# Performance work log

Hardware: AMD Instinct MI355X
Metric: run time of the kernel (lower is better)

Reference implementation:

```python
import jax, jax.numpy as jnp
import numpy as np


def setup_inputs() -> dict:
    key = jax.random.key(0)
    k1, k2 = jax.random.split(key)
    ns, nd, n_classes = 16384, 2048, 1000
    x = jax.random.normal(k1, (ns, nd), dtype=jnp.float32)
    # prototype means for all seen classes (seen_c == n_classes)
    means = jax.random.normal(k2, (n_classes, nd), dtype=jnp.float32)
    return {"x": x, "means": means, "n_classes": n_classes}


def reference(x, means, n_classes):
    # Original: per-sample dist = -means @ x[s]; argmin(dist) == argmax(means @ x[s]).
    # Batched: one GEMM [ns, nd] x [nd, seen_c] -> scores [ns, seen_c].
    ns = x.shape[0]
    xf = x.reshape(ns, -1)
    scores = jnp.einsum('nd,cd->nc', xf, means)  # [ns, seen_c]
    classpred = jnp.argmax(scores, axis=1)       # argmin of -scores
    out = jax.nn.one_hot(classpred, n_classes, dtype=jnp.float32)  # [ns, n_classes]
    return out
```

## Files before the change

kernel.cpp:

```cpp
#include <hip/hip_runtime.h>
#include <math.h>

#define NS 16384
#define ND 2048
#define NC 1000
#define NCPAD 1024

typedef _Float16 f16x8 __attribute__((ext_vector_type(8)));
typedef _Float16 f16x4 __attribute__((ext_vector_type(4)));
typedef __fp16   h16x2 __attribute__((ext_vector_type(2)));
typedef float f32x4  __attribute__((ext_vector_type(4)));

#define DELTA 2.5f

#define WS_NEW 104857600ull
#define WS_MID 37748736ull

__device__ __forceinline__ void gl_lds16_h(const _Float16* g, _Float16* l) {
    __builtin_amdgcn_global_load_lds(
        (const __attribute__((address_space(1))) unsigned int*)g,
        (__attribute__((address_space(3))) unsigned int*)l, 16, 0, 0);
}
__device__ __forceinline__ void gl_lds16_f(const float* g, float* l) {
    __builtin_amdgcn_global_load_lds(
        (const __attribute__((address_space(1))) unsigned int*)g,
        (__attribute__((address_space(3))) unsigned int*)l, 16, 0, 0);
}

__device__ __forceinline__ f16x8 cvt8(const f32x4 a0, const f32x4 a1) {
    const h16x2 h01 = __builtin_amdgcn_cvt_pkrtz(a0[0], a0[1]);
    const h16x2 h23 = __builtin_amdgcn_cvt_pkrtz(a0[2], a0[3]);
    const h16x2 h45 = __builtin_amdgcn_cvt_pkrtz(a1[0], a1[1]);
    const h16x2 h67 = __builtin_amdgcn_cvt_pkrtz(a1[2], a1[3]);
    f16x8 h;
    h[0]=(_Float16)h01[0]; h[1]=(_Float16)h01[1]; h[2]=(_Float16)h23[0]; h[3]=(_Float16)h23[1];
    h[4]=(_Float16)h45[0]; h[5]=(_Float16)h45[1]; h[6]=(_Float16)h67[0]; h[7]=(_Float16)h67[1];
    return h;
}

__global__ __launch_bounds__(256)
void cvt_all_kernel(const float* __restrict__ x, const float* __restrict__ means,
                    _Float16* __restrict__ xh, _Float16* __restrict__ mhi)
{
    const size_t i = (size_t)blockIdx.x * 256 + threadIdx.x;
    const size_t NM4 = (size_t)NCPAD * ND / 4;
    if (i < NM4) {
        const int row = (int)(i >> 9);
        float4 v = make_float4(0.f, 0.f, 0.f, 0.f);
        if (row < NC) v = ((const float4*)means)[i];
        f16x4 h;
        h[0]=(_Float16)v.x; h[1]=(_Float16)v.y; h[2]=(_Float16)v.z; h[3]=(_Float16)v.w;
        ((f16x4*)mhi)[i] = h;
    } else {
        const size_t j = i - NM4;
        const float4 v = ((const float4*)x)[j];
        f16x4 h;
        h[0]=(_Float16)v.x; h[1]=(_Float16)v.y; h[2]=(_Float16)v.z; h[3]=(_Float16)v.w;
        ((f16x4*)xh)[j] = h;
    }
}

__device__ __forceinline__ void stage_unit(const _Float16* __restrict__ src,
                                           size_t g0, _Float16* dstbase,
                                           int ktile, int kkh, int tid)
{
    const int srcT = ktile < 31 ? ktile : 31;
#pragma unroll
    for (int q = 0; q < 2; ++q) {
        const int slot = q * 512 + tid;
        const int row  = slot >> 2;
        const int g    = (slot & 3) ^ ((row >> 1) & 3);
        gl_lds16_h(src + ((g0 + (size_t)row) << 11) + srcT * 64 + kkh * 32 + g * 8,
                   dstbase + (size_t)(q * 512 + ((tid >> 6) << 6)) * 8);
    }
}

__global__ __launch_bounds__(512, 2)
void gemm256_kernel(const _Float16* __restrict__ xh,
                    const _Float16* __restrict__ mhi,
                    _Float16* __restrict__ sc)
{
    __shared__ _Float16 sA[2][2][256 * 32];
    __shared__ _Float16 sB[2][2][256 * 32];

    const int tid  = threadIdx.x;
    const int lane = tid & 63;
    const int w    = tid >> 6;
    const int wm   = w >> 2;
    const int wn   = w & 3;
    const int quad = lane >> 4, l16 = lane & 15;

    const int orig = blockIdx.x + (blockIdx.y << 2);
    const int nid  = ((orig & 7) << 5) + (orig >> 3);
    const size_t gm0 = (size_t)(nid >> 2) * 256;
    const size_t gn0 = (size_t)(nid & 3) * 256;

    f32x4 acc[8][4] = {};

    stage_unit(xh,  gm0, &sA[0][0][0], 0, 0, tid);
    stage_unit(mhi, gn0, &sB[0][0][0], 0, 0, tid);
    stage_unit(xh,  gm0, &sA[0][1][0], 0, 1, tid);
    stage_unit(mhi, gn0, &sB[0][1][0], 0, 1, tid);
    stage_unit(xh,  gm0, &sA[1][0][0], 1, 0, tid);
    stage_unit(mhi, gn0, &sB[1][0][0], 1, 0, tid);
    asm volatile("s_waitcnt vmcnt(4)" ::: "memory");
    __builtin_amdgcn_s_barrier();

    for (int kt = 0; kt < 32; ++kt) {
        const int par = kt & 1;

        f16x8 a0[4], a1[4], b0[4], c0[4], c1[4];
#pragma unroll
        for (int i = 0; i < 4; ++i) {
            const int r0 = wm * 128 + i * 16 + l16;
            const int r1 = r0 + 64;
            const int p0 = quad ^ ((r0 >> 1) & 3);
            const int p1 = quad ^ ((r1 >> 1) & 3);
            a0[i] = *(const f16x8*)&sA[par][0][r0 * 32 + p0 * 8];
            a1[i] = *(const f16x8*)&sA[par][0][r1 * 32 + p1 * 8];
        }
#pragma unroll
        for (int j = 0; j < 4; ++j) {
            const int br = wn * 64 + j * 16 + l16;
            const int pc = quad ^ ((br >> 1) & 3);
            b0[j] = *(const f16x8*)&sB[par][0][br * 32 + pc * 8];
        }
#pragma unroll
        for (int i = 0; i < 4; ++i) {
            const int r0 = wm * 128 + i * 16 + l16;
            const int r1 = r0 + 64;
            const int p0 = quad ^ ((r0 >> 1) & 3);
            const int p1 = quad ^ ((r1 >> 1) & 3);
            c0[i] = *(const f16x8*)&sA[par][1][r0 * 32 + p0 * 8];
            c1[i] = *(const f16x8*)&sA[par][1][r1 * 32 + p1 * 8];
        }
        stage_unit(xh,  gm0, &sA[(kt + 1) & 1][1][0], kt + 1, 1, tid);
        stage_unit(mhi, gn0, &sB[(kt + 1) & 1][1][0], kt + 1, 1, tid);
        __builtin_amdgcn_sched_barrier(0);
        __builtin_amdgcn_s_setprio(1);
#pragma unroll
        for (int i = 0; i < 4; ++i)
#pragma unroll
            for (int j = 0; j < 4; ++j)
                acc[i][j] = __builtin_amdgcn_mfma_f32_16x16x32_f16(a0[i], b0[j], acc[i][j], 0, 0, 0);
#pragma unroll
        for (int i = 0; i < 4; ++i)
#pragma unroll
            for (int j = 0; j < 4; ++j)
                acc[4 + i][j] = __builtin_amdgcn_mfma_f32_16x16x32_f16(a1[i], b0[j], acc[4 + i][j], 0, 0, 0);
        __builtin_amdgcn_s_setprio(0);
        __builtin_amdgcn_s_barrier();

        f16x8 b1[4];
#pragma unroll
        for (int j = 0; j < 4; ++j) {
            const int br = wn * 64 + j * 16 + l16;
            const int pc = quad ^ ((br >> 1) & 3);
            b1[j] = *(const f16x8*)&sB[par][1][br * 32 + pc * 8];
        }
        stage_unit(xh,  gm0, &sA[par][0][0], kt + 2, 0, tid);
        stage_unit(mhi, gn0, &sB[par][0][0], kt + 2, 0, tid);
        __builtin_amdgcn_sched_barrier(0);
        __builtin_amdgcn_s_setprio(1);
#pragma unroll
        for (int i = 0; i < 4; ++i)
#pragma unroll
            for (int j = 0; j < 4; ++j)
                acc[i][j] = __builtin_amdgcn_mfma_f32_16x16x32_f16(c0[i], b1[j], acc[i][j], 0, 0, 0);
#pragma unroll
        for (int i = 0; i < 4; ++i)
#pragma unroll
            for (int j = 0; j < 4; ++j)
                acc[4 + i][j] = __builtin_amdgcn_mfma_f32_16x16x32_f16(c1[i], b1[j], acc[4 + i][j], 0, 0, 0);
        __builtin_amdgcn_s_setprio(0);
        asm volatile("s_waitcnt vmcnt(4)" ::: "memory");
        __builtin_amdgcn_s_barrier();
    }

#pragma unroll
    for (int m = 0; m < 8; ++m) {
        const size_t row0 = gm0 + wm * 128 + m * 16 + quad * 4;
#pragma unroll
        for (int j = 0; j < 4; ++j) {
            const size_t col = gn0 + wn * 64 + j * 16 + l16;
#pragma unroll
            for (int r = 0; r < 4; ++r)
                sc[(row0 + r) * NCPAD + col] = (_Float16)acc[m][j][r];
        }
    }
}

__global__ __launch_bounds__(512, 4)
void gemm_f32a_kernel(const float* __restrict__ x,
                      const _Float16* __restrict__ mhi,
                      _Float16* __restrict__ sc)
{
    __shared__ float    sA [128 * 32];
    __shared__ _Float16 sBh[256 * 32];

    const int tid  = threadIdx.x;
    const int lane = tid & 63;
    const int w    = tid >> 6;
    const int wm   = w & 1;
    const int wn   = w >> 1;
    const int quad = lane >> 4, l16 = lane & 15;
    const size_t gm0 = (size_t)blockIdx.y * 128;
    const size_t gn0 = (size_t)blockIdx.x * 256;

    f32x4 acc[4][4] = {};

    for (int kt = 0; kt < ND / 32; ++kt) {
        const int k0 = kt * 32;
#pragma unroll
        for (int r = 0; r < 2; ++r) {
            const int slot = r * 512 + tid;
            const int arow = slot >> 3;
            const int ac   = (slot & 7) ^ (arow & 7);
            gl_lds16_f(x + ((gm0 + arow) << 11) + k0 + ac * 4,
                       &sA[(r * 512 + w * 64) * 4]);
            const int brow = slot >> 2;
            const int bc   = (slot & 3) ^ ((brow >> 1) & 3);
            gl_lds16_h(mhi + ((gn0 + brow) << 11) + k0 + bc * 8,
                       &sBh[(r * 512 + w * 64) * 8]);
        }
        __syncthreads();

        f16x8 ah[4], bh[4];
#pragma unroll
        for (int i = 0; i < 4; ++i) {
            const int ar = wm * 64 + i * 16 + l16;
            const int c1 = (2 * quad)     ^ (ar & 7);
            const int c2 = (2 * quad + 1) ^ (ar & 7);
            const f32x4 a0 = *(const f32x4*)&sA[ar * 32 + c1 * 4];
            const f32x4 a1 = *(const f32x4*)&sA[ar * 32 + c2 * 4];
            ah[i] = cvt8(a0, a1);
        }
#pragma unroll
        for (int j = 0; j < 4; ++j) {
            const int br = wn * 64 + j * 16 + l16;
            const int pc = quad ^ ((br >> 1) & 3);
            bh[j] = *(const f16x8*)&sBh[br * 32 + pc * 8];
        }
#pragma unroll
        for (int i = 0; i < 4; ++i)
#pragma unroll
            for (int j = 0; j < 4; ++j)
                acc[i][j] = __builtin_amdgcn_mfma_f32_16x16x32_f16(ah[i], bh[j], acc[i][j], 0, 0, 0);
        __syncthreads();
    }

#pragma unroll
    for (int i = 0; i < 4; ++i) {
        const size_t row0 = gm0 + wm * 64 + i * 16 + quad * 4;
#pragma unroll
        for (int j = 0; j < 4; ++j) {
            const size_t col = gn0 + wn * 64 + j * 16 + l16;
#pragma unroll
            for (int r = 0; r < 4; ++r)
                sc[(row0 + r) * NCPAD + col] = (_Float16)acc[i][j][r];
        }
    }
}

__global__ __launch_bounds__(256)
void cvt_m_kernel(const float* __restrict__ src, _Float16* __restrict__ hi)
{
    const int i = blockIdx.x * 256 + threadIdx.x;
    const int row = (i * 4) >> 11;
    float4 v = make_float4(0.f, 0.f, 0.f, 0.f);
    if (row < NC) v = ((const float4*)src)[i];
    f16x4 h;
    h[0] = (_Float16)v.x; h[1] = (_Float16)v.y;
    h[2] = (_Float16)v.z; h[3] = (_Float16)v.w;
    ((f16x4*)hi)[i] = h;
}

__global__ __launch_bounds__(256, 4)
void refine_kernel(const _Float16* __restrict__ sc,
                   const float* __restrict__ x,
                   const float* __restrict__ means,
                   float* __restrict__ out)
{
    const int lane = threadIdx.x & 63;
    const int row  = blockIdx.x * 4 + (threadIdx.x >> 6);

    const f16x8* srow = (const f16x8*)(sc + (size_t)row * NCPAD + lane * 16);
    const f16x8 s0 = srow[0], s1 = srow[1];
    float v[16];
#pragma unroll
    for (int e = 0; e < 8; ++e) { v[e] = (float)s0[e]; v[8 + e] = (float)s1[e]; }

    float mx = -INFINITY;
#pragma unroll
    for (int e = 0; e < 16; ++e) {
        const int c = lane * 16 + e;
        if (c < NC && v[e] > mx) mx = v[e];
    }
#pragma unroll
    for (int off = 1; off < 64; off <<= 1) {
        const float o = __shfl_xor(mx, off);
        if (o > mx) mx = o;
    }
    const float T = mx - DELTA;

    unsigned cm = 0;
#pragma unroll
    for (int e = 0; e < 16; ++e) {
        const int c = lane * 16 + e;
        if (c < NC && v[e] >= T) cm |= (1u << e);
    }

    const unsigned long long bl = __ballot(cm != 0u);
    const int first  = (int)__builtin_ctzll(bl);
    const unsigned cmf = (unsigned)__shfl((int)cm, first);

    int bc;
    if (__builtin_popcountll(bl) == 1 && __builtin_popcount(cmf) == 1) {
        bc = first * 16 + __builtin_ctz(cmf);
    } else {
        const float* xrow = x + ((size_t)row << 11);
        f32x4 xr[8];
#pragma unroll
        for (int it = 0; it < 8; ++it)
            xr[it] = *(const f32x4*)(xrow + it * 256 + lane * 4);

        float bv = -INFINITY;
        bc = 0x7fffffff;
        unsigned long long pend = bl;
        while (pend) {
            const int src = (int)__builtin_ctzll(pend);
            pend &= pend - 1;
            unsigned cms = (unsigned)__shfl((int)cm, src);
            while (cms) {
                const int c = src * 16 + __builtin_ctz(cms);
                cms &= cms - 1;

                const float* mrow = means + ((size_t)c << 11);
                float part = 0.f;
#pragma unroll
                for (int it = 0; it < 8; ++it) {
                    const f32x4 mv = *(const f32x4*)(mrow + it * 256 + lane * 4);
                    part = fmaf(xr[it][0], mv[0], part);
                    part = fmaf(xr[it][1], mv[1], part);
                    part = fmaf(xr[it][2], mv[2], part);
                    part = fmaf(xr[it][3], mv[3], part);
                }
                float s = part;
#pragma unroll
                for (int off = 1; off < 64; off <<= 1) s += __shfl_xor(s, off);

                if (s > bv || (s == bv && c < bc)) { bv = s; bc = c; }
            }
        }
    }

    float4* orow = (float4*)(out + (size_t)row * NC);
#pragma unroll
    for (int i = 0; i < 4; ++i) {
        const int idx = lane + i * 64;
        if (idx < NC / 4) {
            const int cb = idx * 4;
            float4 ov;
            ov.x = (cb     == bc) ? 1.f : 0.f;
            ov.y = (cb + 1 == bc) ? 1.f : 0.f;
            ov.z = (cb + 2 == bc) ? 1.f : 0.f;
            ov.w = (cb + 3 == bc) ? 1.f : 0.f;
            orow[idx] = ov;
        }
    }
}

#define MS 64
#define CS 256
#define KT 32
#define NCHUNK 4

__global__ __launch_bounds__(256, 1)
void nnc_fp32_kernel(const float* __restrict__ x,
                     const float* __restrict__ means,
                     float* __restrict__ out)
{
    __shared__ float xs[MS * KT];
    __shared__ float msh[CS * KT];
    __shared__ float rbest[MS * 33];
    __shared__ int   ridx[MS * 33];
    __shared__ int   widx[MS];

    const int tid = threadIdx.x;
    const int tx  = tid & 31;
    const int ty  = tid >> 5;
    const int s0  = blockIdx.x * MS;
    const int m0  = ty * 8;
    const int cL  = tx * 8;

    float best[8];
    int   bidx[8];
#pragma unroll
    for (int i = 0; i < 8; ++i) { best[i] = -INFINITY; bidx[i] = 0; }

    const int kslot = tid & 7;
    const int rrow  = tid >> 3;

    for (int chunk = 0; chunk < NCHUNK; ++chunk) {
        const int c0 = chunk * CS;
        float acc[8][8];
#pragma unroll
        for (int i = 0; i < 8; ++i)
#pragma unroll
            for (int j = 0; j < 8; ++j) acc[i][j] = 0.0f;

        for (int k0 = 0; k0 < ND; k0 += KT) {
#pragma unroll
            for (int r = 0; r < 2; ++r) {
                const int m = rrow + r * 32;
                const float4 v = *(const float4*)(x + (size_t)(s0 + m) * ND + k0 + kslot * 4);
                *(float4*)(xs + m * KT + kslot * 4) = v;
            }
#pragma unroll
            for (int r = 0; r < 8; ++r) {
                const int c  = rrow + r * 32;
                const int cg = c0 + c;
                float4 v = make_float4(0.f, 0.f, 0.f, 0.f);
                if (cg < NC) v = *(const float4*)(means + (size_t)cg * ND + k0 + kslot * 4);
                const int pslot = (kslot + (c >> 3)) & 7;
                *(float4*)(msh + c * KT + pslot * 4) = v;
            }
            __syncthreads();
#pragma unroll
            for (int k4 = 0; k4 < KT / 4; ++k4) {
                float4 a[8], b[8];
                const int boff = ((k4 + tx) & 7) * 4;
#pragma unroll
                for (int i = 0; i < 8; ++i) a[i] = *(const float4*)(xs + (m0 + i) * KT + k4 * 4);
#pragma unroll
                for (int j = 0; j < 8; ++j) b[j] = *(const float4*)(msh + (cL + j) * KT + boff);
#pragma unroll
                for (int i = 0; i < 8; ++i)
#pragma unroll
                    for (int j = 0; j < 8; ++j) {
                        acc[i][j] = fmaf(a[i].x, b[j].x, acc[i][j]);
                        acc[i][j] = fmaf(a[i].y, b[j].y, acc[i][j]);
                        acc[i][j] = fmaf(a[i].z, b[j].z, acc[i][j]);
                        acc[i][j] = fmaf(a[i].w, b[j].w, acc[i][j]);
                    }
            }
            __syncthreads();
        }
#pragma unroll
        for (int i = 0; i < 8; ++i)
#pragma unroll
            for (int j = 0; j < 8; ++j) {
                const int c = c0 + cL + j;
                const float v = acc[i][j];
                if (c < NC && (v > best[i] || (v == best[i] && c < bidx[i]))) {
                    best[i] = v; bidx[i] = c;
                }
            }
    }
#pragma unroll
    for (int i = 0; i < 8; ++i) {
        rbest[(m0 + i) * 33 + tx] = best[i];
        ridx[(m0 + i) * 33 + tx]  = bidx[i];
    }
    __syncthreads();
    if (tid < MS) {
        float bv = rbest[tid * 33];
        int   bc = ridx[tid * 33];
        for (int t = 1; t < 32; ++t) {
            const float v = rbest[tid * 33 + t];
            const int   c = ridx[tid * 33 + t];
            if (v > bv || (v == bv && c < bc)) { bv = v; bc = c; }
        }
        widx[tid] = bc;
    }
    __syncthreads();
    if (tid < 250) {
        const int cbase = tid * 4;
        for (int m = 0; m < MS; ++m) {
            const int w = widx[m];
            float4 v;
            v.x = (cbase == w) ? 1.f : 0.f;
            v.y = (cbase + 1 == w) ? 1.f : 0.f;
            v.z = (cbase + 2 == w) ? 1.f : 0.f;
            v.w = (cbase + 3 == w) ? 1.f : 0.f;
            *(float4*)(out + (size_t)(s0 + m) * NC + cbase) = v;
        }
    }
}

extern "C" void kernel_launch(void* const* d_in, const int* in_sizes, int n_in,
                              void* d_out, int out_size, void* d_ws, size_t ws_size,
                              hipStream_t stream) {
    const float* x     = (const float*)d_in[0];
    const float* means = (const float*)d_in[1];
    float* out         = (float*)d_out;

    if (ws_size >= WS_NEW) {
        char* ws = (char*)d_ws;
        _Float16* mhi = (_Float16*)ws;
        _Float16* xh  = (_Float16*)(ws + (4ull  << 20));
        _Float16* sc  = (_Float16*)(ws + (68ull << 20));

        cvt_all_kernel<<<dim3((NCPAD * ND / 4 + NS * ND / 4) / 256), dim3(256), 0, stream>>>(x, means, xh, mhi);
        gemm256_kernel<<<dim3(NCPAD / 256, NS / 256), dim3(512), 0, stream>>>(xh, mhi, sc);
        refine_kernel<<<dim3(NS / 4), dim3(256), 0, stream>>>(sc, x, means, out);
    } else if (ws_size >= WS_MID) {
        char* ws = (char*)d_ws;
        _Float16* mhi = (_Float16*)ws;
        _Float16* sc  = (_Float16*)(ws + 4194304ull);

        cvt_m_kernel<<<dim3(NCPAD * ND / 4 / 256), dim3(256), 0, stream>>>(means, mhi);
        gemm_f32a_kernel<<<dim3(NCPAD / 256, NS / 128), dim3(512), 0, stream>>>(x, mhi, sc);
        refine_kernel<<<dim3(NS / 4), dim3(256), 0, stream>>>(sc, x, means, out);
    } else {
        nnc_fp32_kernel<<<dim3(NS / MS), dim3(256), 0, stream>>>(x, means, out);
    }
}
```

Baseline: 301.8 us.

## Fuse fp32-to-fp16 conversion of x into the 256x256 GEMM A-tile load

Removes the separate pass that converted all of x to fp16 in workspace. The 256x256 GEMM now loads fp32 x straight from global memory into registers, converts it to fp16 and writes the swizzled tile into LDS, while B still arrives through direct global-to-LDS loads. This saves writing and re-reading a 64 MB fp16 copy of x and needs less workspace. In exchange, the A path costs VGPRs and conversion ALU work inside the MFMA loop, and the loop now waits on vmcnt(0) every iteration instead of keeping loads in flight.

```diff
diff --git a/kernel.cpp b/kernel.cpp
--- a/kernel.cpp
+++ b/kernel.cpp
@@ -13,15 +13,9 @@
 
 #define DELTA 2.5f
 
-#define WS_NEW 104857600ull
-#define WS_MID 37748736ull
+#define WS_FAST 37748736ull
 
 __device__ __forceinline__ void gl_lds16_h(const _Float16* g, _Float16* l) {
-    __builtin_amdgcn_global_load_lds(
-        (const __attribute__((address_space(1))) unsigned int*)g,
-        (__attribute__((address_space(3))) unsigned int*)l, 16, 0, 0);
-}
-__device__ __forceinline__ void gl_lds16_f(const float* g, float* l) {
     __builtin_amdgcn_global_load_lds(
         (const __attribute__((address_space(1))) unsigned int*)g,
         (__attribute__((address_space(3))) unsigned int*)l, 16, 0, 0);
@@ -36,230 +30,6 @@
     h[0]=(_Float16)h01[0]; h[1]=(_Float16)h01[1]; h[2]=(_Float16)h23[0]; h[3]=(_Float16)h23[1];
     h[4]=(_Float16)h45[0]; h[5]=(_Float16)h45[1]; h[6]=(_Float16)h67[0]; h[7]=(_Float16)h67[1];
     return h;
-}
-
-__global__ __launch_bounds__(256)
-void cvt_all_kernel(const float* __restrict__ x, const float* __restrict__ means,
-                    _Float16* __restrict__ xh, _Float16* __restrict__ mhi)
-{
-    const size_t i = (size_t)blockIdx.x * 256 + threadIdx.x;
-    const size_t NM4 = (size_t)NCPAD * ND / 4;
-    if (i < NM4) {
-        const int row = (int)(i >> 9);
-        float4 v = make_float4(0.f, 0.f, 0.f, 0.f);
-        if (row < NC) v = ((const float4*)means)[i];
-        f16x4 h;
-        h[0]=(_Float16)v.x; h[1]=(_Float16)v.y; h[2]=(_Float16)v.z; h[3]=(_Float16)v.w;
-        ((f16x4*)mhi)[i] = h;
-    } else {
-        const size_t j = i - NM4;
-        const float4 v = ((const float4*)x)[j];
-        f16x4 h;
-        h[0]=(_Float16)v.x; h[1]=(_Float16)v.y; h[2]=(_Float16)v.z; h[3]=(_Float16)v.w;
-        ((f16x4*)xh)[j] = h;
-    }
-}
-
-__device__ __forceinline__ void stage_unit(const _Float16* __restrict__ src,
-                                           size_t g0, _Float16* dstbase,
-                                           int ktile, int kkh, int tid)
-{
-    const int srcT = ktile < 31 ? ktile : 31;
-#pragma unroll
-    for (int q = 0; q < 2; ++q) {
-        const int slot = q * 512 + tid;
-        const int row  = slot >> 2;
-        const int g    = (slot & 3) ^ ((row >> 1) & 3);
-        gl_lds16_h(src + ((g0 + (size_t)row) << 11) + srcT * 64 + kkh * 32 + g * 8,
-                   dstbase + (size_t)(q * 512 + ((tid >> 6) << 6)) * 8);
-    }
-}
-
-__global__ __launch_bounds__(512, 2)
-void gemm256_kernel(const _Float16* __restrict__ xh,
-                    const _Float16* __restrict__ mhi,
-                    _Float16* __restrict__ sc)
-{
-    __shared__ _Float16 sA[2][2][256 * 32];
-    __shared__ _Float16 sB[2][2][256 * 32];
-
-    const int tid  = threadIdx.x;
-    const int lane = tid & 63;
-    const int w    = tid >> 6;
-    const int wm   = w >> 2;
-    const int wn   = w & 3;
-    const int quad = lane >> 4, l16 = lane & 15;
-
-    const int orig = blockIdx.x + (blockIdx.y << 2);
-    const int nid  = ((orig & 7) << 5) + (orig >> 3);
-    const size_t gm0 = (size_t)(nid >> 2) * 256;
-    const size_t gn0 = (size_t)(nid & 3) * 256;
-
-    f32x4 acc[8][4] = {};
-
-    stage_unit(xh,  gm0, &sA[0][0][0], 0, 0, tid);
-    stage_unit(mhi, gn0, &sB[0][0][0], 0, 0, tid);
-    stage_unit(xh,  gm0, &sA[0][1][0], 0, 1, tid);
-    stage_unit(mhi, gn0, &sB[0][1][0], 0, 1, tid);
-    stage_unit(xh,  gm0, &sA[1][0][0], 1, 0, tid);
-    stage_unit(mhi, gn0, &sB[1][0][0], 1, 0, tid);
-    asm volatile("s_waitcnt vmcnt(4)" ::: "memory");
-    __builtin_amdgcn_s_barrier();
-
-    for (int kt = 0; kt < 32; ++kt) {
-        const int par = kt & 1;
-
-        f16x8 a0[4], a1[4], b0[4], c0[4], c1[4];
-#pragma unroll
-        for (int i = 0; i < 4; ++i) {
-            const int r0 = wm * 128 + i * 16 + l16;
-            const int r1 = r0 + 64;
-            const int p0 = quad ^ ((r0 >> 1) & 3);
-            const int p1 = quad ^ ((r1 >> 1) & 3);
-            a0[i] = *(const f16x8*)&sA[par][0][r0 * 32 + p0 * 8];
-            a1[i] = *(const f16x8*)&sA[par][0][r1 * 32 + p1 * 8];
-        }
-#pragma unroll
-        for (int j = 0; j < 4; ++j) {
-            const int br = wn * 64 + j * 16 + l16;
-            const int pc = quad ^ ((br >> 1) & 3);
-            b0[j] = *(const f16x8*)&sB[par][0][br * 32 + pc * 8];
-        }
-#pragma unroll
-        for (int i = 0; i < 4; ++i) {
-            const int r0 = wm * 128 + i * 16 + l16;
-            const int r1 = r0 + 64;
-            const int p0 = quad ^ ((r0 >> 1) & 3);
-            const int p1 = quad ^ ((r1 >> 1) & 3);
-            c0[i] = *(const f16x8*)&sA[par][1][r0 * 32 + p0 * 8];
-            c1[i] = *(const f16x8*)&sA[par][1][r1 * 32 + p1 * 8];
-        }
-        stage_unit(xh,  gm0, &sA[(kt + 1) & 1][1][0], kt + 1, 1, tid);
-        stage_unit(mhi, gn0, &sB[(kt + 1) & 1][1][0], kt + 1, 1, tid);
-        __builtin_amdgcn_sched_barrier(0);
-        __builtin_amdgcn_s_setprio(1);
-#pragma unroll
-        for (int i = 0; i < 4; ++i)
-#pragma unroll
-            for (int j = 0; j < 4; ++j)
-                acc[i][j] = __builtin_amdgcn_mfma_f32_16x16x32_f16(a0[i], b0[j], acc[i][j], 0, 0, 0);
-#pragma unroll
-        for (int i = 0; i < 4; ++i)
-#pragma unroll
-            for (int j = 0; j < 4; ++j)
-                acc[4 + i][j] = __builtin_amdgcn_mfma_f32_16x16x32_f16(a1[i], b0[j], acc[4 + i][j], 0, 0, 0);
-        __builtin_amdgcn_s_setprio(0);
-        __builtin_amdgcn_s_barrier();
-
-        f16x8 b1[4];
-#pragma unroll
-        for (int j = 0; j < 4; ++j) {
-            const int br = wn * 64 + j * 16 + l16;
-            const int pc = quad ^ ((br >> 1) & 3);
-            b1[j] = *(const f16x8*)&sB[par][1][br * 32 + pc * 8];
-        }
-        stage_unit(xh,  gm0, &sA[par][0][0], kt + 2, 0, tid);
-        stage_unit(mhi, gn0, &sB[par][0][0], kt + 2, 0, tid);
-        __builtin_amdgcn_sched_barrier(0);
-        __builtin_amdgcn_s_setprio(1);
-#pragma unroll
-        for (int i = 0; i < 4; ++i)
-#pragma unroll
-            for (int j = 0; j < 4; ++j)
-                acc[i][j] = __builtin_amdgcn_mfma_f32_16x16x32_f16(c0[i], b1[j], acc[i][j], 0, 0, 0);
-#pragma unroll
-        for (int i = 0; i < 4; ++i)
-#pragma unroll
-            for (int j = 0; j < 4; ++j)
-                acc[4 + i][j] = __builtin_amdgcn_mfma_f32_16x16x32_f16(c1[i], b1[j], acc[4 + i][j], 0, 0, 0);
-        __builtin_amdgcn_s_setprio(0);
-        asm volatile("s_waitcnt vmcnt(4)" ::: "memory");
-        __builtin_amdgcn_s_barrier();
-    }
-
-#pragma unroll
-    for (int m = 0; m < 8; ++m) {
-        const size_t row0 = gm0 + wm * 128 + m * 16 + quad * 4;
-#pragma unroll
-        for (int j = 0; j < 4; ++j) {
-            const size_t col = gn0 + wn * 64 + j * 16 + l16;
-#pragma unroll
-            for (int r = 0; r < 4; ++r)
-                sc[(row0 + r) * NCPAD + col] = (_Float16)acc[m][j][r];
-        }
-    }
-}
-
-__global__ __launch_bounds__(512, 4)
-void gemm_f32a_kernel(const float* __restrict__ x,
-                      const _Float16* __restrict__ mhi,
-                      _Float16* __restrict__ sc)
-{
-    __shared__ float    sA [128 * 32];
-    __shared__ _Float16 sBh[256 * 32];
-
-    const int tid  = threadIdx.x;
-    const int lane = tid & 63;
-    const int w    = tid >> 6;
-    const int wm   = w & 1;
-    const int wn   = w >> 1;
-    const int quad = lane >> 4, l16 = lane & 15;
-    const size_t gm0 = (size_t)blockIdx.y * 128;
-    const size_t gn0 = (size_t)blockIdx.x * 256;
-
-    f32x4 acc[4][4] = {};
-
-    for (int kt = 0; kt < ND / 32; ++kt) {
-        const int k0 = kt * 32;
-#pragma unroll
-        for (int r = 0; r < 2; ++r) {
-            const int slot = r * 512 + tid;
-            const int arow = slot >> 3;
-            const int ac   = (slot & 7) ^ (arow & 7);
-            gl_lds16_f(x + ((gm0 + arow) << 11) + k0 + ac * 4,
-                       &sA[(r * 512 + w * 64) * 4]);
-            const int brow = slot >> 2;
-            const int bc   = (slot & 3) ^ ((brow >> 1) & 3);
-            gl_lds16_h(mhi + ((gn0 + brow) << 11) + k0 + bc * 8,
-                       &sBh[(r * 512 + w * 64) * 8]);
-        }
-        __syncthreads();
-
-        f16x8 ah[4], bh[4];
-#pragma unroll
-        for (int i = 0; i < 4; ++i) {
-            const int ar = wm * 64 + i * 16 + l16;
-            const int c1 = (2 * quad)     ^ (ar & 7);
-            const int c2 = (2 * quad + 1) ^ (ar & 7);
-            const f32x4 a0 = *(const f32x4*)&sA[ar * 32 + c1 * 4];
-            const f32x4 a1 = *(const f32x4*)&sA[ar * 32 + c2 * 4];
-            ah[i] = cvt8(a0, a1);
-        }
-#pragma unroll
-        for (int j = 0; j < 4; ++j) {
-            const int br = wn * 64 + j * 16 + l16;
-            const int pc = quad ^ ((br >> 1) & 3);
-            bh[j] = *(const f16x8*)&sBh[br * 32 + pc * 8];
-        }
-#pragma unroll
-        for (int i = 0; i < 4; ++i)
-#pragma unroll
-            for (int j = 0; j < 4; ++j)
-                acc[i][j] = __builtin_amdgcn_mfma_f32_16x16x32_f16(ah[i], bh[j], acc[i][j], 0, 0, 0);
-        __syncthreads();
-    }
-
-#pragma unroll
-    for (int i = 0; i < 4; ++i) {
-        const size_t row0 = gm0 + wm * 64 + i * 16 + quad * 4;
-#pragma unroll
-        for (int j = 0; j < 4; ++j) {
-            const size_t col = gn0 + wn * 64 + j * 16 + l16;
-#pragma unroll
-            for (int r = 0; r < 4; ++r)
-                sc[(row0 + r) * NCPAD + col] = (_Float16)acc[i][j][r];
-        }
-    }
 }
 
 __global__ __launch_bounds__(256)
@@ -275,6 +45,160 @@
     ((f16x4*)hi)[i] = h;
 }
 
+__device__ __forceinline__ void stage_unitB(const _Float16* __restrict__ src,
+                                            size_t g0, _Float16* dstbase,
+                                            int srcT, int kkh, int tid)
+{
+#pragma unroll
+    for (int q = 0; q < 2; ++q) {
+        const int slot = q * 512 + tid;
+        const int row  = slot >> 2;
+        const int g    = (slot & 3) ^ ((row >> 1) & 3);
+        gl_lds16_h(src + ((g0 + (size_t)row) << 11) + srcT * 64 + kkh * 32 + g * 8,
+                   dstbase + (size_t)(q * 512 + ((tid >> 6) << 6)) * 8);
+    }
+}
+
+__global__ __launch_bounds__(512, 2)
+void gemm256_kernel(const float* __restrict__ x,
+                    const _Float16* __restrict__ mhi,
+                    _Float16* __restrict__ sc)
+{
+    __shared__ _Float16 sA[2][2][256 * 32];
+    __shared__ _Float16 sB[2][2][256 * 32];
+
+    const int tid  = threadIdx.x;
+    const int lane = tid & 63;
+    const int w    = tid >> 6;
+    const int wm   = w >> 2;
+    const int wn   = w & 3;
+    const int quad = lane >> 4, l16 = lane & 15;
+
+    const int orig = blockIdx.x + (blockIdx.y << 2);
+    const int nid  = ((orig & 7) << 5) + (orig >> 3);
+    const size_t gm0 = (size_t)(nid >> 2) * 256;
+    const size_t gn0 = (size_t)(nid & 3) * 256;
+
+    const int arow = tid >> 1;
+    const int aseg = tid & 1;
+    const int as   = (arow >> 1) & 3;
+    const int ap0  = (aseg * 2)     ^ as;
+    const int ap1  = (aseg * 2 + 1) ^ as;
+    const float* xA = x + ((gm0 + (size_t)arow) << 11) + aseg * 16;
+
+    f32x4 acc[8][4] = {};
+
+    stage_unitB(mhi, gn0, &sB[0][0][0], 0, 0, tid);
+    stage_unitB(mhi, gn0, &sB[0][1][0], 0, 1, tid);
+    {
+        f32x4 v0[4], v1[4];
+#pragma unroll
+        for (int q = 0; q < 4; ++q) v0[q] = *(const f32x4*)(xA + q * 4);
+#pragma unroll
+        for (int q = 0; q < 4; ++q) v1[q] = *(const f32x4*)(xA + 32 + q * 4);
+        const f16x8 h00 = cvt8(v0[0], v0[1]), h01 = cvt8(v0[2], v0[3]);
+        const f16x8 h10 = cvt8(v1[0], v1[1]), h11 = cvt8(v1[2], v1[3]);
+        *(f16x8*)&sA[0][0][arow * 32 + ap0 * 8] = h00;
+        *(f16x8*)&sA[0][0][arow * 32 + ap1 * 8] = h01;
+        *(f16x8*)&sA[0][1][arow * 32 + ap0 * 8] = h10;
+        *(f16x8*)&sA[0][1][arow * 32 + ap1 * 8] = h11;
+    }
+    asm volatile("s_waitcnt vmcnt(0) lgkmcnt(0)" ::: "memory");
+    __builtin_amdgcn_s_barrier();
+
+    for (int kt = 0; kt < 32; ++kt) {
+        const int par = kt & 1, nxt = par ^ 1;
+        const int srcT = (kt + 1 < 32) ? kt + 1 : 31;
+        const float* xT = xA + srcT * 64;
+
+        f16x8 a0[4], a1[4], b0[4];
+#pragma unroll
+        for (int i = 0; i < 4; ++i) {
+            const int r0 = wm * 128 + i * 16 + l16;
+            const int r1 = r0 + 64;
+            a0[i] = *(const f16x8*)&sA[par][0][r0 * 32 + (quad ^ ((r0 >> 1) & 3)) * 8];
+            a1[i] = *(const f16x8*)&sA[par][0][r1 * 32 + (quad ^ ((r1 >> 1) & 3)) * 8];
+        }
+#pragma unroll
+        for (int j = 0; j < 4; ++j) {
+            const int br = wn * 64 + j * 16 + l16;
+            b0[j] = *(const f16x8*)&sB[par][0][br * 32 + (quad ^ ((br >> 1) & 3)) * 8];
+        }
+        stage_unitB(mhi, gn0, &sB[nxt][0][0], srcT, 0, tid);
+        stage_unitB(mhi, gn0, &sB[nxt][1][0], srcT, 1, tid);
+        f32x4 av0[4];
+#pragma unroll
+        for (int q = 0; q < 4; ++q) av0[q] = *(const f32x4*)(xT + q * 4);
+        __builtin_amdgcn_sched_barrier(0);
+        __builtin_amdgcn_s_setprio(1);
+#pragma unroll
+        for (int i = 0; i < 4; ++i)
+#pragma unroll
+            for (int j = 0; j < 4; ++j)
+                acc[i][j] = __builtin_amdgcn_mfma_f32_16x16x32_f16(a0[i], b0[j], acc[i][j], 0, 0, 0);
+#pragma unroll
+        for (int i = 0; i < 4; ++i)
+#pragma unroll
+            for (int j = 0; j < 4; ++j)
+                acc[4 + i][j] = __builtin_amdgcn_mfma_f32_16x16x32_f16(a1[i], b0[j], acc[4 + i][j], 0, 0, 0);
+        __builtin_amdgcn_s_setprio(0);
+
+        f16x8 c0[4], c1[4], b1[4];
+#pragma unroll
+        for (int i = 0; i < 4; ++i) {
+            const int r0 = wm * 128 + i * 16 + l16;
+            const int r1 = r0 + 64;
+            c0[i] = *(const f16x8*)&sA[par][1][r0 * 32 + (quad ^ ((r0 >> 1) & 3)) * 8];
+            c1[i] = *(const f16x8*)&sA[par][1][r1 * 32 + (quad ^ ((r1 >> 1) & 3)) * 8];
+        }
+#pragma unroll
+        for (int j = 0; j < 4; ++j) {
+            const int br = wn * 64 + j * 16 + l16;
+            b1[j] = *(const f16x8*)&sB[par][1][br * 32 + (quad ^ ((br >> 1) & 3)) * 8];
+        }
+        {
+            const f16x8 h0 = cvt8(av0[0], av0[1]), h1 = cvt8(av0[2], av0[3]);
+            *(f16x8*)&sA[nxt][0][arow * 32 + ap0 * 8] = h0;
+            *(f16x8*)&sA[nxt][0][arow * 32 + ap1 * 8] = h1;
+        }
+        f32x4 av1[4];
+#pragma unroll
+        for (int q = 0; q < 4; ++q) av1[q] = *(const f32x4*)(xT + 32 + q * 4);
+        __builtin_amdgcn_sched_barrier(0);
+        __builtin_amdgcn_s_setprio(1);
+#pragma unroll
+        for (int i = 0; i < 4; ++i)
+#pragma unroll
+            for (int j = 0; j < 4; ++j)
+                acc[i][j] = __builtin_amdgcn_mfma_f32_16x16x32_f16(c0[i], b1[j], acc[i][j], 0, 0, 0);
+#pragma unroll
+        for (int i = 0; i < 4; ++i)
+#pragma unroll
+            for (int j = 0; j < 4; ++j)
+                acc[4 + i][j] = __builtin_amdgcn_mfma_f32_16x16x32_f16(c1[i], b1[j], acc[4 + i][j], 0, 0, 0);
+        __builtin_amdgcn_s_setprio(0);
+        {
+            const f16x8 h0 = cvt8(av1[0], av1[1]), h1 = cvt8(av1[2], av1[3]);
+            *(f16x8*)&sA[nxt][1][arow * 32 + ap0 * 8] = h0;
+            *(f16x8*)&sA[nxt][1][arow * 32 + ap1 * 8] = h1;
+        }
+        asm volatile("s_waitcnt vmcnt(0) lgkmcnt(0)" ::: "memory");
+        __builtin_amdgcn_s_barrier();
+    }
+
+#pragma unroll
+    for (int m = 0; m < 8; ++m) {
+        const size_t row0 = gm0 + wm * 128 + m * 16 + quad * 4;
+#pragma unroll
+        for (int j = 0; j < 4; ++j) {
+            const size_t col = gn0 + wn * 64 + j * 16 + l16;
+#pragma unroll
+            for (int r = 0; r < 4; ++r)
+                sc[(row0 + r) * NCPAD + col] = (_Float16)acc[m][j][r];
+        }
+    }
+}
+
 __global__ __launch_bounds__(256, 4)
 void refine_kernel(const _Float16* __restrict__ sc,
                    const float* __restrict__ x,
@@ -495,22 +419,13 @@
     const float* means = (const float*)d_in[1];
     float* out         = (float*)d_out;
 
-    if (ws_size >= WS_NEW) {
+    if (ws_size >= WS_FAST) {
         char* ws = (char*)d_ws;
         _Float16* mhi = (_Float16*)ws;
-        _Float16* xh  = (_Float16*)(ws + (4ull  << 20));
-        _Float16* sc  = (_Float16*)(ws + (68ull << 20));
-
-        cvt_all_kernel<<<dim3((NCPAD * ND / 4 + NS * ND / 4) / 256), dim3(256), 0, stream>>>(x, means, xh, mhi);
-        gemm256_kernel<<<dim3(NCPAD / 256, NS / 256), dim3(512), 0, stream>>>(xh, mhi, sc);
-        refine_kernel<<<dim3(NS / 4), dim3(256), 0, stream>>>(sc, x, means, out);
-    } else if (ws_size >= WS_MID) {
-        char* ws = (char*)d_ws;
-        _Float16* mhi = (_Float16*)ws;
-        _Float16* sc  = (_Float16*)(ws + 4194304ull);
+        _Float16* sc  = (_Float16*)(ws + (4ull << 20));
 
         cvt_m_kernel<<<dim3(NCPAD * ND / 4 / 256), dim3(256), 0, stream>>>(means, mhi);
-        gemm_f32a_kernel<<<dim3(NCPAD / 256, NS / 128), dim3(512), 0, stream>>>(x, mhi, sc);
+        gemm256_kernel<<<dim3(NCPAD / 256, NS / 256), dim3(512), 0, stream>>>(x, mhi, sc);
         refine_kernel<<<dim3(NS / 4), dim3(256), 0, stream>>>(sc, x, means, out);
     } else {
         nnc_fp32_kernel<<<dim3(NS / MS), dim3(256), 0, stream>>>(x, means, out);
```

Measured after the change: 306.3 us. About the same (+1.5%).
